# Kernel tuning notes

Hardware: AMD Instinct MI355X
Metric: run time of the kernel (lower is better)

The kernel has to match this reference:

```python
import jax, jax.numpy as jnp
import numpy as np

D = 768
N_GROUPS = 4
KEYS_PER_Q = 4 * 196  # 784


def setup_inputs() -> dict:
    key = jax.random.key(0)
    ks = jax.random.split(key, 6)
    scale = 0.02
    return {
        "LR_image": jax.random.normal(ks[0], (N_GROUPS, 32, D), jnp.float32),
        "HR_image": jax.random.normal(ks[1], (N_GROUPS, 32 * KEYS_PER_Q, D), jnp.float32),
        "Wq": jax.random.normal(ks[2], (D, D), jnp.float32) * scale,
        "bq": jnp.zeros((D,), jnp.float32),
        "Wk": jax.random.normal(ks[3], (D, D), jnp.float32) * scale,
        "bk": jnp.zeros((D,), jnp.float32),
        "Wv": jax.random.normal(ks[4], (D, D), jnp.float32) * scale,
        "bv": jnp.zeros((D,), jnp.float32),
        "Wo": jax.random.normal(ks[5], (D, D), jnp.float32) * scale,
        "bo": jnp.zeros((D,), jnp.float32),
        "gamma": jnp.ones((D,), jnp.float32),
        "beta": jnp.zeros((D,), jnp.float32),
    }


def reference(LR_image, HR_image, Wq, bq, Wk, bk, Wv, bv, Wo, bo, gamma, beta):
    d = LR_image.shape[-1]
    # version == 2 reshapes from the original forward
    lr = LR_image.reshape(1, -1, 32, 1, d)            # [1, N, 32, 1, D]
    hr = HR_image.reshape(1, -1, 32, KEYS_PER_Q, d)   # [1, N, 32, 784, D]
    q = lr @ Wq.T + bq                                # [1, N, 32, 1, D]
    k = hr @ Wk.T + bk                                # [1, N, 32, 784, D]
    v = hr @ Wv.T + bv
    # single-head attention; query_len == 1, key_len == 784
    scores = jnp.einsum('bnsqd,bnskd->bnsqk', q, k) / jnp.sqrt(jnp.float32(d))
    p = jax.nn.softmax(scores, axis=-1)               # dropout = identity (eval)
    x = jnp.einsum('bnsqk,bnskd->bnsqd', p, v)        # [1, N, 32, 1, D]
    x = x.reshape(1, -1, d)                           # [1, N*32, D]
    q = q.reshape(1, -1, d)
    x = x @ Wo.T + bo
    y = q + x                                         # residual (dropout_2 = identity)
    mu = jnp.mean(y, axis=-1, keepdims=True)
    var = jnp.mean((y - mu) ** 2, axis=-1, keepdims=True)
    return (y - mu) * jax.lax.rsqrt(var + 1e-5) * gamma + beta
```

## Files before the change

kernel.cpp:

```cpp
#include <hip/hip_runtime.h>
#include <math.h>

#define D 768
#define DF2 384
#define DF4 192
#define NQ 128
#define KPQ 784
#define NCHUNK 16
#define KCHUNK 49

#define EXP2F(x) __builtin_amdgcn_exp2f(x)

__device__ __forceinline__ float dot4f(const float4 a, const float4 b) {
    return a.x * b.x + a.y * b.y + a.z * b.z + a.w * b.w;
}

__global__ __launch_bounds__(256) void k_tr(const float* __restrict__ Wq,
                                            const float* __restrict__ Wv,
                                            const float* __restrict__ Wo,
                                            float* __restrict__ WqT,
                                            float* __restrict__ WvT,
                                            float* __restrict__ WoT) {
    __shared__ float t[64][65];
    const float* src;
    float* dst;
    if (blockIdx.y == 0)      { src = Wq; dst = WqT; }
    else if (blockIdx.y == 1) { src = Wv; dst = WvT; }
    else                      { src = Wo; dst = WoT; }
    const int tr = blockIdx.x / 12, tc = blockIdx.x % 12;
    const int r0 = tr * 64, c0 = tc * 64;
    const int lr = threadIdx.x >> 6, lc = threadIdx.x & 63;
#pragma unroll
    for (int i = 0; i < 16; ++i)
        t[lr + i * 4][lc] = src[(size_t)(r0 + lr + i * 4) * D + c0 + lc];
    __syncthreads();
#pragma unroll
    for (int i = 0; i < 16; ++i)
        dst[(size_t)(c0 + lr + i * 4) * D + r0 + lc] = t[lc][lr + i * 4];
}

template <bool BIAS, bool RES>
__global__ __launch_bounds__(512) void k_gemm2(const float* __restrict__ A,
                                               const float2* __restrict__ W2,
                                               const float2* __restrict__ bias2,
                                               const float2* __restrict__ res2,
                                               float2* __restrict__ Out2) {
    __shared__ float2 part[8][4][64];
    const int ct  = blockIdx.x % 6;
    const int q0  = (blockIdx.x / 6) * 4;
    const int tid = threadIdx.x;
    const int ds  = __builtin_amdgcn_readfirstlane(tid >> 6);
    const int c2  = tid & 63;
    const int e2  = ct * 64 + c2;
    const float* a0 = A + (size_t)q0 * D;
    const float* a1 = a0 + D;
    const float* a2 = a1 + D;
    const float* a3 = a2 + D;
    float2 acc0 = {0.f, 0.f}, acc1 = {0.f, 0.f}, acc2 = {0.f, 0.f}, acc3 = {0.f, 0.f};
    const int dbase = ds * 96;
#pragma unroll 8
    for (int i = 0; i < 96; ++i) {
        const int d = dbase + i;
        const float2 wv = W2[(size_t)d * DF2 + e2];
        const float x0 = a0[d], x1 = a1[d], x2 = a2[d], x3 = a3[d];
        acc0.x = fmaf(x0, wv.x, acc0.x); acc0.y = fmaf(x0, wv.y, acc0.y);
        acc1.x = fmaf(x1, wv.x, acc1.x); acc1.y = fmaf(x1, wv.y, acc1.y);
        acc2.x = fmaf(x2, wv.x, acc2.x); acc2.y = fmaf(x2, wv.y, acc2.y);
        acc3.x = fmaf(x3, wv.x, acc3.x); acc3.y = fmaf(x3, wv.y, acc3.y);
    }
    part[ds][0][c2] = acc0;
    part[ds][1][c2] = acc1;
    part[ds][2][c2] = acc2;
    part[ds][3][c2] = acc3;
    __syncthreads();
    if (tid < 256) {
        const int q = tid >> 6, c = tid & 63;
        float2 s = {0.f, 0.f};
#pragma unroll
        for (int p = 0; p < 8; ++p) {
            s.x += part[p][q][c].x;
            s.y += part[p][q][c].y;
        }
        if (BIAS) {
            const float2 b = bias2[ct * 64 + c];
            s.x += b.x; s.y += b.y;
        }
        if (RES) {
            const float2 r = res2[(size_t)(q0 + q) * DF2 + ct * 64 + c];
            s.x += r.x; s.y += r.y;
        }
        Out2[(size_t)(q0 + q) * DF2 + ct * 64 + c] = s;
    }
}

__global__ __launch_bounds__(256) void k_flash(const float4* __restrict__ HR,
                                               const float4* __restrict__ qt,
                                               float4* __restrict__ Cpart,
                                               float* __restrict__ Lp) {
    const int b     = blockIdx.x;
    const int qi    = b >> 4;
    const int chunk = b & 15;
    const size_t rowbase = (size_t)qi * KPQ + (size_t)chunk * KCHUNK;
    const int tid  = threadIdx.x;
    const int w    = tid >> 6;
    const int lane = tid & 63;

    const float rsd2 = 0.036084391824351615f * 1.4426950408889634f;
    float4 qa = qt[qi * DF4 + lane];
    float4 qb = qt[qi * DF4 + lane + 64];
    float4 qc = qt[qi * DF4 + lane + 128];
    qa.x *= rsd2; qa.y *= rsd2; qa.z *= rsd2; qa.w *= rsd2;
    qb.x *= rsd2; qb.y *= rsd2; qb.z *= rsd2; qb.w *= rsd2;
    qc.x *= rsd2; qc.y *= rsd2; qc.z *= rsd2; qc.w *= rsd2;

    float l = 0.f;
    float4 c0 = make_float4(0.f, 0.f, 0.f, 0.f);
    float4 c1 = make_float4(0.f, 0.f, 0.f, 0.f);
    float4 c2 = make_float4(0.f, 0.f, 0.f, 0.f);

    int j = w;
    while (j + 4 < KCHUNK) {
        const float4* rowA = HR + (rowbase + (size_t)j) * DF4;
        const float4* rowB = HR + (rowbase + (size_t)(j + 4)) * DF4;
        const float4 a0 = rowA[lane], a1 = rowA[lane + 64], a2 = rowA[lane + 128];
        const float4 b0 = rowB[lane], b1 = rowB[lane + 64], b2 = rowB[lane + 128];
        float p1 = dot4f(qa, a0) + dot4f(qb, a1) + dot4f(qc, a2);
        float p2 = dot4f(qa, b0) + dot4f(qb, b1) + dot4f(qc, b2);
#pragma unroll
        for (int off = 32; off; off >>= 1) {
            p1 += __shfl_xor(p1, off, 64);
            p2 += __shfl_xor(p2, off, 64);
        }
        const float e1 = EXP2F(p1);
        const float e2 = EXP2F(p2);
        l += e1 + e2;
        c0.x += fmaf(e1, a0.x, e2 * b0.x);
        c0.y += fmaf(e1, a0.y, e2 * b0.y);
        c0.z += fmaf(e1, a0.z, e2 * b0.z);
        c0.w += fmaf(e1, a0.w, e2 * b0.w);
        c1.x += fmaf(e1, a1.x, e2 * b1.x);
        c1.y += fmaf(e1, a1.y, e2 * b1.y);
        c1.z += fmaf(e1, a1.z, e2 * b1.z);
        c1.w += fmaf(e1, a1.w, e2 * b1.w);
        c2.x += fmaf(e1, a2.x, e2 * b2.x);
        c2.y += fmaf(e1, a2.y, e2 * b2.y);
        c2.z += fmaf(e1, a2.z, e2 * b2.z);
        c2.w += fmaf(e1, a2.w, e2 * b2.w);
        j += 8;
    }
    if (j < KCHUNK) {
        const float4* rowA = HR + (rowbase + (size_t)j) * DF4;
        const float4 a0 = rowA[lane], a1 = rowA[lane + 64], a2 = rowA[lane + 128];
        float p1 = dot4f(qa, a0) + dot4f(qb, a1) + dot4f(qc, a2);
#pragma unroll
        for (int off = 32; off; off >>= 1) p1 += __shfl_xor(p1, off, 64);
        const float e1 = EXP2F(p1);
        l += e1;
        c0.x = fmaf(e1, a0.x, c0.x); c0.y = fmaf(e1, a0.y, c0.y);
        c0.z = fmaf(e1, a0.z, c0.z); c0.w = fmaf(e1, a0.w, c0.w);
        c1.x = fmaf(e1, a1.x, c1.x); c1.y = fmaf(e1, a1.y, c1.y);
        c1.z = fmaf(e1, a1.z, c1.z); c1.w = fmaf(e1, a1.w, c1.w);
        c2.x = fmaf(e1, a2.x, c2.x); c2.y = fmaf(e1, a2.y, c2.y);
        c2.z = fmaf(e1, a2.z, c2.z); c2.w = fmaf(e1, a2.w, c2.w);
    }

    __shared__ __align__(16) float4 c_lds[4][DF4];
    __shared__ float l_lds[4];
    c_lds[w][lane]       = c0;
    c_lds[w][lane + 64]  = c1;
    c_lds[w][lane + 128] = c2;
    if (lane == 0) l_lds[w] = l;
    __syncthreads();

    if (tid < DF4) {
        float4 cc = make_float4(0.f, 0.f, 0.f, 0.f);
#pragma unroll
        for (int p = 0; p < 4; ++p) {
            const float4 cv = c_lds[p][tid];
            cc.x += cv.x; cc.y += cv.y; cc.z += cv.z; cc.w += cv.w;
        }
        Cpart[(size_t)b * DF4 + tid] = cc;
        if (tid == 0) Lp[b] = l_lds[0] + l_lds[1] + l_lds[2] + l_lds[3];
    }
}

__global__ __launch_bounds__(192) void k_combine(const float4* __restrict__ Cpart,
                                                 const float* __restrict__ Lp,
                                                 float4* __restrict__ Cn) {
    const int qi = blockIdx.x;
    const int f  = threadIdx.x;
    float L = 0.f;
#pragma unroll
    for (int p = 0; p < NCHUNK; ++p) L += Lp[qi * NCHUNK + p];
    float4 c = make_float4(0.f, 0.f, 0.f, 0.f);
#pragma unroll
    for (int p = 0; p < NCHUNK; ++p) {
        const float4 v = Cpart[(size_t)(qi * NCHUNK + p) * DF4 + f];
        c.x += v.x; c.y += v.y; c.z += v.z; c.w += v.w;
    }
    const float inv = 1.f / L;
    c.x *= inv; c.y *= inv; c.z *= inv; c.w *= inv;
    Cn[(size_t)qi * DF4 + f] = c;
}

__global__ __launch_bounds__(256) void k_ln(const float* __restrict__ y,
                                            const float* __restrict__ gamma,
                                            const float* __restrict__ beta,
                                            float* __restrict__ out) {
    __shared__ float sp[4], ssp[4];
    const int qi = blockIdx.x;
    const int tid = threadIdx.x, w = tid >> 6, lane = tid & 63;
    const float* yr = y + (size_t)qi * D;
    const float v0 = yr[tid], v1 = yr[tid + 256], v2 = yr[tid + 512];
    float s  = v0 + v1 + v2;
    float ss = v0 * v0 + v1 * v1 + v2 * v2;
#pragma unroll
    for (int off = 32; off; off >>= 1) {
        s  += __shfl_xor(s, off, 64);
        ss += __shfl_xor(ss, off, 64);
    }
    if (lane == 0) { sp[w] = s; ssp[w] = ss; }
    __syncthreads();
    s  = sp[0] + sp[1] + sp[2] + sp[3];
    ss = ssp[0] + ssp[1] + ssp[2] + ssp[3];
    const float mu  = s * (1.f / 768.f);
    const float var = ss * (1.f / 768.f) - mu * mu;
    const float rs  = rsqrtf(var + 1e-5f);
    float* o = out + (size_t)qi * D;
    o[tid]       = (v0 - mu) * rs * gamma[tid]       + beta[tid];
    o[tid + 256] = (v1 - mu) * rs * gamma[tid + 256] + beta[tid + 256];
    o[tid + 512] = (v2 - mu) * rs * gamma[tid + 512] + beta[tid + 512];
}

extern "C" void kernel_launch(void* const* d_in, const int* in_sizes, int n_in,
                              void* d_out, int out_size, void* d_ws, size_t ws_size,
                              hipStream_t stream) {
    const float* LR    = (const float*)d_in[0];
    const float* HR    = (const float*)d_in[1];
    const float* Wq    = (const float*)d_in[2];
    const float* bq    = (const float*)d_in[3];
    const float* Wk    = (const float*)d_in[4];
    const float* Wv    = (const float*)d_in[6];
    const float* bv    = (const float*)d_in[7];
    const float* Wo    = (const float*)d_in[8];
    const float* bo    = (const float*)d_in[9];
    const float* gamma = (const float*)d_in[10];
    const float* beta  = (const float*)d_in[11];
    float* out = (float*)d_out;

    float* ws = (float*)d_ws;
    float* WqT   = ws;
    float* WvT   = ws + 589824;
    float* WoT   = ws + 1179648;
    float* qbuf  = ws + 1769472;
    float* qtbuf = ws + 1867776;
    float* Cpart = ws + 1966080;
    float* Lp    = ws + 3538944;
    float* Cn    = ws + 3540992;
    float* Xbuf  = ws + 3639296;
    float* ybuf  = ws + 3737600;

    k_tr<<<dim3(144, 3), 256, 0, stream>>>(Wq, Wv, Wo, WqT, WvT, WoT);
    k_gemm2<true, false><<<192, 512, 0, stream>>>(LR, (const float2*)WqT,
                                                  (const float2*)bq, nullptr,
                                                  (float2*)qbuf);
    k_gemm2<false, false><<<192, 512, 0, stream>>>(qbuf, (const float2*)Wk,
                                                   nullptr, nullptr,
                                                   (float2*)qtbuf);
    k_flash<<<NQ * NCHUNK, 256, 0, stream>>>((const float4*)HR, (const float4*)qtbuf,
                                             (float4*)Cpart, Lp);
    k_combine<<<NQ, 192, 0, stream>>>((const float4*)Cpart, Lp, (float4*)Cn);
    k_gemm2<true, false><<<192, 512, 0, stream>>>(Cn, (const float2*)WvT,
                                                  (const float2*)bv, nullptr,
                                                  (float2*)Xbuf);
    k_gemm2<true, true><<<192, 512, 0, stream>>>(Xbuf, (const float2*)WoT,
                                                 (const float2*)bo, (const float2*)qbuf,
                                                 (float2*)ybuf);
    k_ln<<<NQ, 256, 0, stream>>>(ybuf, gamma, beta, out);
}
```

Measured before the change: 104.5 us.

## Fuse Q and Q·Wk projections, and fold chunk combine into the V GEMM

The Q projection and the Wk projection of q are merged into one kernel. Each column-tile block computes its slice of q and then a split-K partial of q·Wk, and the six partials are summed and scaled inside the flash kernel's prologue. The separate combine kernel is removed: the V-projection GEMM now reduces the chunk partials and sums itself, applying 1/L in its epilogue. This cuts two kernel launches and their intermediate round trips, in exchange for redundant partial reductions across column-tile blocks and extra partial buffers.

```diff
diff --git a/kernel.cpp b/kernel.cpp
--- a/kernel.cpp
+++ b/kernel.cpp
@@ -8,6 +8,7 @@
 #define KPQ 784
 #define NCHUNK 16
 #define KCHUNK 49
+#define NCT 6
 
 #define EXP2F(x) __builtin_amdgcn_exp2f(x)
 
@@ -39,8 +40,264 @@
         dst[(size_t)(c0 + lr + i * 4) * D + r0 + lc] = t[lc][lr + i * 4];
 }
 
-template <bool BIAS, bool RES>
-__global__ __launch_bounds__(512) void k_gemm2(const float* __restrict__ A,
+__global__ __launch_bounds__(512) void k_gqqt(const float* __restrict__ LR,
+                                              const float2* __restrict__ WqT2,
+                                              const float2* __restrict__ bq2,
+                                              const float2* __restrict__ Wk2,
+                                              float* __restrict__ qbuf,
+                                              float2* __restrict__ qtp2) {
+    __shared__ float2 part[8][4][64];
+    const int ct  = blockIdx.x;
+    const int q0  = blockIdx.y * 4;
+    const int tid = threadIdx.x;
+    const int wid = __builtin_amdgcn_readfirstlane(tid >> 6);
+    const int c2  = tid & 63;
+
+    {
+        const int e2 = ct * 64 + c2;
+        const float* a0 = LR + (size_t)q0 * D;
+        const float* a1 = a0 + D;
+        const float* a2 = a1 + D;
+        const float* a3 = a2 + D;
+        float2 acc0 = {0.f, 0.f}, acc1 = {0.f, 0.f}, acc2 = {0.f, 0.f}, acc3 = {0.f, 0.f};
+        const int cbase = wid * 96;
+#pragma unroll 8
+        for (int i = 0; i < 96; ++i) {
+            const int c = cbase + i;
+            const float2 wv = WqT2[(size_t)c * DF2 + e2];
+            const float x0 = a0[c], x1 = a1[c], x2 = a2[c], x3 = a3[c];
+            acc0.x = fmaf(x0, wv.x, acc0.x); acc0.y = fmaf(x0, wv.y, acc0.y);
+            acc1.x = fmaf(x1, wv.x, acc1.x); acc1.y = fmaf(x1, wv.y, acc1.y);
+            acc2.x = fmaf(x2, wv.x, acc2.x); acc2.y = fmaf(x2, wv.y, acc2.y);
+            acc3.x = fmaf(x3, wv.x, acc3.x); acc3.y = fmaf(x3, wv.y, acc3.y);
+        }
+        part[wid][0][c2] = acc0;
+        part[wid][1][c2] = acc1;
+        part[wid][2][c2] = acc2;
+        part[wid][3][c2] = acc3;
+    }
+    __syncthreads();
+    if (tid < 256) {
+        const int q = tid >> 6, c = tid & 63;
+        float2 s = {0.f, 0.f};
+#pragma unroll
+        for (int p = 0; p < 8; ++p) {
+            s.x += part[p][q][c].x;
+            s.y += part[p][q][c].y;
+        }
+        const float2 b = bq2[ct * 64 + c];
+        s.x += b.x; s.y += b.y;
+        *reinterpret_cast<float2*>(&qbuf[(size_t)(q0 + q) * D + (ct * 64 + c) * 2]) = s;
+    }
+    __syncthreads();
+
+    if (wid < 6) {
+        const int ee2 = wid * 64 + (tid & 63);
+        float2 b0 = {0.f, 0.f}, b1 = {0.f, 0.f}, b2 = {0.f, 0.f}, b3 = {0.f, 0.f};
+        const int dbase = ct * 128;
+        for (int i4 = 0; i4 < 32; ++i4) {
+            const int d = dbase + i4 * 4;
+            const float4 x0 = *reinterpret_cast<const float4*>(&qbuf[(size_t)(q0 + 0) * D + d]);
+            const float4 x1 = *reinterpret_cast<const float4*>(&qbuf[(size_t)(q0 + 1) * D + d]);
+            const float4 x2 = *reinterpret_cast<const float4*>(&qbuf[(size_t)(q0 + 2) * D + d]);
+            const float4 x3 = *reinterpret_cast<const float4*>(&qbuf[(size_t)(q0 + 3) * D + d]);
+#pragma unroll
+            for (int k = 0; k < 4; ++k) {
+                const float2 wv = Wk2[(size_t)(d + k) * DF2 + ee2];
+                const float v0 = (k == 0) ? x0.x : (k == 1) ? x0.y : (k == 2) ? x0.z : x0.w;
+                const float v1 = (k == 0) ? x1.x : (k == 1) ? x1.y : (k == 2) ? x1.z : x1.w;
+                const float v2 = (k == 0) ? x2.x : (k == 1) ? x2.y : (k == 2) ? x2.z : x2.w;
+                const float v3 = (k == 0) ? x3.x : (k == 1) ? x3.y : (k == 2) ? x3.z : x3.w;
+                b0.x = fmaf(v0, wv.x, b0.x); b0.y = fmaf(v0, wv.y, b0.y);
+                b1.x = fmaf(v1, wv.x, b1.x); b1.y = fmaf(v1, wv.y, b1.y);
+                b2.x = fmaf(v2, wv.x, b2.x); b2.y = fmaf(v2, wv.y, b2.y);
+                b3.x = fmaf(v3, wv.x, b3.x); b3.y = fmaf(v3, wv.y, b3.y);
+            }
+        }
+        qtp2[(size_t)(ct * NQ + q0 + 0) * DF2 + ee2] = b0;
+        qtp2[(size_t)(ct * NQ + q0 + 1) * DF2 + ee2] = b1;
+        qtp2[(size_t)(ct * NQ + q0 + 2) * DF2 + ee2] = b2;
+        qtp2[(size_t)(ct * NQ + q0 + 3) * DF2 + ee2] = b3;
+    }
+}
+
+__global__ __launch_bounds__(256) void k_flash(const float4* __restrict__ HR,
+                                               const float4* __restrict__ qtp4,
+                                               float4* __restrict__ Cpart,
+                                               float* __restrict__ Lp) {
+    __shared__ __align__(16) float4 qt_lds[DF4];
+    const int b     = blockIdx.x;
+    const int qi    = b >> 4;
+    const int chunk = b & 15;
+    const size_t rowbase = (size_t)qi * KPQ + (size_t)chunk * KCHUNK;
+    const int tid  = threadIdx.x;
+    const int w    = tid >> 6;
+    const int lane = tid & 63;
+
+    if (tid < DF4) {
+        float4 s = make_float4(0.f, 0.f, 0.f, 0.f);
+#pragma unroll
+        for (int ct = 0; ct < NCT; ++ct) {
+            const float4 v = qtp4[(size_t)(ct * NQ + qi) * DF4 + tid];
+            s.x += v.x; s.y += v.y; s.z += v.z; s.w += v.w;
+        }
+        const float rsd2 = 0.036084391824351615f * 1.4426950408889634f;
+        s.x *= rsd2; s.y *= rsd2; s.z *= rsd2; s.w *= rsd2;
+        qt_lds[tid] = s;
+    }
+    __syncthreads();
+
+    const float4 qa = qt_lds[lane];
+    const float4 qb = qt_lds[lane + 64];
+    const float4 qc = qt_lds[lane + 128];
+
+    float l = 0.f;
+    float4 c0 = make_float4(0.f, 0.f, 0.f, 0.f);
+    float4 c1 = make_float4(0.f, 0.f, 0.f, 0.f);
+    float4 c2 = make_float4(0.f, 0.f, 0.f, 0.f);
+
+    int j = w;
+    while (j + 4 < KCHUNK) {
+        const float4* rowA = HR + (rowbase + (size_t)j) * DF4;
+        const float4* rowB = HR + (rowbase + (size_t)(j + 4)) * DF4;
+        const float4 a0 = rowA[lane], a1 = rowA[lane + 64], a2 = rowA[lane + 128];
+        const float4 b0 = rowB[lane], b1 = rowB[lane + 64], b2 = rowB[lane + 128];
+        float p1 = dot4f(qa, a0) + dot4f(qb, a1) + dot4f(qc, a2);
+        float p2 = dot4f(qa, b0) + dot4f(qb, b1) + dot4f(qc, b2);
+#pragma unroll
+        for (int off = 32; off; off >>= 1) {
+            p1 += __shfl_xor(p1, off, 64);
+            p2 += __shfl_xor(p2, off, 64);
+        }
+        const float e1 = EXP2F(p1);
+        const float e2 = EXP2F(p2);
+        l += e1 + e2;
+        c0.x += fmaf(e1, a0.x, e2 * b0.x);
+        c0.y += fmaf(e1, a0.y, e2 * b0.y);
+        c0.z += fmaf(e1, a0.z, e2 * b0.z);
+        c0.w += fmaf(e1, a0.w, e2 * b0.w);
+        c1.x += fmaf(e1, a1.x, e2 * b1.x);
+        c1.y += fmaf(e1, a1.y, e2 * b1.y);
+        c1.z += fmaf(e1, a1.z, e2 * b1.z);
+        c1.w += fmaf(e1, a1.w, e2 * b1.w);
+        c2.x += fmaf(e1, a2.x, e2 * b2.x);
+        c2.y += fmaf(e1, a2.y, e2 * b2.y);
+        c2.z += fmaf(e1, a2.z, e2 * b2.z);
+        c2.w += fmaf(e1, a2.w, e2 * b2.w);
+        j += 8;
+    }
+    if (j < KCHUNK) {
+        const float4* rowA = HR + (rowbase + (size_t)j) * DF4;
+        const float4 a0 = rowA[lane], a1 = rowA[lane + 64], a2 = rowA[lane + 128];
+        float p1 = dot4f(qa, a0) + dot4f(qb, a1) + dot4f(qc, a2);
+#pragma unroll
+        for (int off = 32; off; off >>= 1) p1 += __shfl_xor(p1, off, 64);
+        const float e1 = EXP2F(p1);
+        l += e1;
+        c0.x = fmaf(e1, a0.x, c0.x); c0.y = fmaf(e1, a0.y, c0.y);
+        c0.z = fmaf(e1, a0.z, c0.z); c0.w = fmaf(e1, a0.w, c0.w);
+        c1.x = fmaf(e1, a1.x, c1.x); c1.y = fmaf(e1, a1.y, c1.y);
+        c1.z = fmaf(e1, a1.z, c1.z); c1.w = fmaf(e1, a1.w, c1.w);
+        c2.x = fmaf(e1, a2.x, c2.x); c2.y = fmaf(e1, a2.y, c2.y);
+        c2.z = fmaf(e1, a2.z, c2.z); c2.w = fmaf(e1, a2.w, c2.w);
+    }
+
+    __shared__ __align__(16) float4 c_lds[4][DF4];
+    __shared__ float l_lds[4];
+    c_lds[w][lane]       = c0;
+    c_lds[w][lane + 64]  = c1;
+    c_lds[w][lane + 128] = c2;
+    if (lane == 0) l_lds[w] = l;
+    __syncthreads();
+
+    if (tid < DF4) {
+        float4 cc = make_float4(0.f, 0.f, 0.f, 0.f);
+#pragma unroll
+        for (int p = 0; p < 4; ++p) {
+            const float4 cv = c_lds[p][tid];
+            cc.x += cv.x; cc.y += cv.y; cc.z += cv.z; cc.w += cv.w;
+        }
+        Cpart[(size_t)b * DF4 + tid] = cc;
+        if (tid == 0) Lp[b] = l_lds[0] + l_lds[1] + l_lds[2] + l_lds[3];
+    }
+}
+
+__global__ __launch_bounds__(512) void k_gemmV(const float4* __restrict__ Cpart4,
+                                               const float* __restrict__ Lp,
+                                               const float2* __restrict__ WvT2,
+                                               const float2* __restrict__ bv2,
+                                               float* __restrict__ cnbuf,
+                                               float2* __restrict__ Xbuf2) {
+    __shared__ float2 part[8][4][64];
+    const int ct  = blockIdx.x;
+    const int q0  = blockIdx.y * 4;
+    const int tid = threadIdx.x;
+
+    for (int f = tid; f < 4 * DF4; f += 512) {
+        const int q = f / DF4, ff = f % DF4;
+        float4 s = make_float4(0.f, 0.f, 0.f, 0.f);
+#pragma unroll
+        for (int p = 0; p < NCHUNK; ++p) {
+            const float4 v = Cpart4[(size_t)((q0 + q) * NCHUNK + p) * DF4 + ff];
+            s.x += v.x; s.y += v.y; s.z += v.z; s.w += v.w;
+        }
+        *reinterpret_cast<float4*>(&cnbuf[(size_t)(q0 + q) * D + ff * 4]) = s;
+    }
+    float invL[4];
+#pragma unroll
+    for (int q = 0; q < 4; ++q) {
+        float L = 0.f;
+#pragma unroll
+        for (int p = 0; p < NCHUNK; ++p) L += Lp[(q0 + q) * NCHUNK + p];
+        invL[q] = 1.f / L;
+    }
+    __syncthreads();
+
+    const int wid = __builtin_amdgcn_readfirstlane(tid >> 6);
+    const int c2  = tid & 63;
+    const int e2  = ct * 64 + c2;
+    float2 acc0 = {0.f, 0.f}, acc1 = {0.f, 0.f}, acc2 = {0.f, 0.f}, acc3 = {0.f, 0.f};
+    const int dbase = wid * 96;
+    for (int i4 = 0; i4 < 24; ++i4) {
+        const int d = dbase + i4 * 4;
+        const float4 x0 = *reinterpret_cast<const float4*>(&cnbuf[(size_t)(q0 + 0) * D + d]);
+        const float4 x1 = *reinterpret_cast<const float4*>(&cnbuf[(size_t)(q0 + 1) * D + d]);
+        const float4 x2 = *reinterpret_cast<const float4*>(&cnbuf[(size_t)(q0 + 2) * D + d]);
+        const float4 x3 = *reinterpret_cast<const float4*>(&cnbuf[(size_t)(q0 + 3) * D + d]);
+#pragma unroll
+        for (int k = 0; k < 4; ++k) {
+            const float2 wv = WvT2[(size_t)(d + k) * DF2 + e2];
+            const float v0 = (k == 0) ? x0.x : (k == 1) ? x0.y : (k == 2) ? x0.z : x0.w;
+            const float v1 = (k == 0) ? x1.x : (k == 1) ? x1.y : (k == 2) ? x1.z : x1.w;
+            const float v2 = (k == 0) ? x2.x : (k == 1) ? x2.y : (k == 2) ? x2.z : x2.w;
+            const float v3 = (k == 0) ? x3.x : (k == 1) ? x3.y : (k == 2) ? x3.z : x3.w;
+            acc0.x = fmaf(v0, wv.x, acc0.x); acc0.y = fmaf(v0, wv.y, acc0.y);
+            acc1.x = fmaf(v1, wv.x, acc1.x); acc1.y = fmaf(v1, wv.y, acc1.y);
+            acc2.x = fmaf(v2, wv.x, acc2.x); acc2.y = fmaf(v2, wv.y, acc2.y);
+            acc3.x = fmaf(v3, wv.x, acc3.x); acc3.y = fmaf(v3, wv.y, acc3.y);
+        }
+    }
+    part[wid][0][c2] = acc0;
+    part[wid][1][c2] = acc1;
+    part[wid][2][c2] = acc2;
+    part[wid][3][c2] = acc3;
+    __syncthreads();
+    if (tid < 256) {
+        const int q = tid >> 6, c = tid & 63;
+        float2 s = {0.f, 0.f};
+#pragma unroll
+        for (int p = 0; p < 8; ++p) {
+            s.x += part[p][q][c].x;
+            s.y += part[p][q][c].y;
+        }
+        const float2 b = bv2[ct * 64 + c];
+        s.x = s.x * invL[q] + b.x;
+        s.y = s.y * invL[q] + b.y;
+        Xbuf2[(size_t)(q0 + q) * DF2 + ct * 64 + c] = s;
+    }
+}
+
+__global__ __launch_bounds__(512) void k_gemmO(const float* __restrict__ A,
                                                const float2* __restrict__ W2,
                                                const float2* __restrict__ bias2,
                                                const float2* __restrict__ res2,
@@ -81,126 +338,12 @@
             s.x += part[p][q][c].x;
             s.y += part[p][q][c].y;
         }
-        if (BIAS) {
-            const float2 b = bias2[ct * 64 + c];
-            s.x += b.x; s.y += b.y;
-        }
-        if (RES) {
-            const float2 r = res2[(size_t)(q0 + q) * DF2 + ct * 64 + c];
-            s.x += r.x; s.y += r.y;
-        }
+        const float2 b = bias2[ct * 64 + c];
+        const float2 r = res2[(size_t)(q0 + q) * DF2 + ct * 64 + c];
+        s.x += b.x + r.x;
+        s.y += b.y + r.y;
         Out2[(size_t)(q0 + q) * DF2 + ct * 64 + c] = s;
     }
-}
-
-__global__ __launch_bounds__(256) void k_flash(const float4* __restrict__ HR,
-                                               const float4* __restrict__ qt,
-                                               float4* __restrict__ Cpart,
-                                               float* __restrict__ Lp) {
-    const int b     = blockIdx.x;
-    const int qi    = b >> 4;
-    const int chunk = b & 15;
-    const size_t rowbase = (size_t)qi * KPQ + (size_t)chunk * KCHUNK;
-    const int tid  = threadIdx.x;
-    const int w    = tid >> 6;
-    const int lane = tid & 63;
-
-    const float rsd2 = 0.036084391824351615f * 1.4426950408889634f;
-    float4 qa = qt[qi * DF4 + lane];
-    float4 qb = qt[qi * DF4 + lane + 64];
-    float4 qc = qt[qi * DF4 + lane + 128];
-    qa.x *= rsd2; qa.y *= rsd2; qa.z *= rsd2; qa.w *= rsd2;
-    qb.x *= rsd2; qb.y *= rsd2; qb.z *= rsd2; qb.w *= rsd2;
-    qc.x *= rsd2; qc.y *= rsd2; qc.z *= rsd2; qc.w *= rsd2;
-
-    float l = 0.f;
-    float4 c0 = make_float4(0.f, 0.f, 0.f, 0.f);
-    float4 c1 = make_float4(0.f, 0.f, 0.f, 0.f);
-    float4 c2 = make_float4(0.f, 0.f, 0.f, 0.f);
-
-    int j = w;
-    while (j + 4 < KCHUNK) {
-        const float4* rowA = HR + (rowbase + (size_t)j) * DF4;
-        const float4* rowB = HR + (rowbase + (size_t)(j + 4)) * DF4;
-        const float4 a0 = rowA[lane], a1 = rowA[lane + 64], a2 = rowA[lane + 128];
-        const float4 b0 = rowB[lane], b1 = rowB[lane + 64], b2 = rowB[lane + 128];
-        float p1 = dot4f(qa, a0) + dot4f(qb, a1) + dot4f(qc, a2);
-        float p2 = dot4f(qa, b0) + dot4f(qb, b1) + dot4f(qc, b2);
-#pragma unroll
-        for (int off = 32; off; off >>= 1) {
-            p1 += __shfl_xor(p1, off, 64);
-            p2 += __shfl_xor(p2, off, 64);
-        }
-        const float e1 = EXP2F(p1);
-        const float e2 = EXP2F(p2);
-        l += e1 + e2;
-        c0.x += fmaf(e1, a0.x, e2 * b0.x);
-        c0.y += fmaf(e1, a0.y, e2 * b0.y);
-        c0.z += fmaf(e1, a0.z, e2 * b0.z);
-        c0.w += fmaf(e1, a0.w, e2 * b0.w);
-        c1.x += fmaf(e1, a1.x, e2 * b1.x);
-        c1.y += fmaf(e1, a1.y, e2 * b1.y);
-        c1.z += fmaf(e1, a1.z, e2 * b1.z);
-        c1.w += fmaf(e1, a1.w, e2 * b1.w);
-        c2.x += fmaf(e1, a2.x, e2 * b2.x);
-        c2.y += fmaf(e1, a2.y, e2 * b2.y);
-        c2.z += fmaf(e1, a2.z, e2 * b2.z);
-        c2.w += fmaf(e1, a2.w, e2 * b2.w);
-        j += 8;
-    }
-    if (j < KCHUNK) {
-        const float4* rowA = HR + (rowbase + (size_t)j) * DF4;
-        const float4 a0 = rowA[lane], a1 = rowA[lane + 64], a2 = rowA[lane + 128];
-        float p1 = dot4f(qa, a0) + dot4f(qb, a1) + dot4f(qc, a2);
-#pragma unroll
-        for (int off = 32; off; off >>= 1) p1 += __shfl_xor(p1, off, 64);
-        const float e1 = EXP2F(p1);
-        l += e1;
-        c0.x = fmaf(e1, a0.x, c0.x); c0.y = fmaf(e1, a0.y, c0.y);
-        c0.z = fmaf(e1, a0.z, c0.z); c0.w = fmaf(e1, a0.w, c0.w);
-        c1.x = fmaf(e1, a1.x, c1.x); c1.y = fmaf(e1, a1.y, c1.y);
-        c1.z = fmaf(e1, a1.z, c1.z); c1.w = fmaf(e1, a1.w, c1.w);
-        c2.x = fmaf(e1, a2.x, c2.x); c2.y = fmaf(e1, a2.y, c2.y);
-        c2.z = fmaf(e1, a2.z, c2.z); c2.w = fmaf(e1, a2.w, c2.w);
-    }
-
-    __shared__ __align__(16) float4 c_lds[4][DF4];
-    __shared__ float l_lds[4];
-    c_lds[w][lane]       = c0;
-    c_lds[w][lane + 64]  = c1;
-    c_lds[w][lane + 128] = c2;
-    if (lane == 0) l_lds[w] = l;
-    __syncthreads();
-
-    if (tid < DF4) {
-        float4 cc = make_float4(0.f, 0.f, 0.f, 0.f);
-#pragma unroll
-        for (int p = 0; p < 4; ++p) {
-            const float4 cv = c_lds[p][tid];
-            cc.x += cv.x; cc.y += cv.y; cc.z += cv.z; cc.w += cv.w;
-        }
-        Cpart[(size_t)b * DF4 + tid] = cc;
-        if (tid == 0) Lp[b] = l_lds[0] + l_lds[1] + l_lds[2] + l_lds[3];
-    }
-}
-
-__global__ __launch_bounds__(192) void k_combine(const float4* __restrict__ Cpart,
-                                                 const float* __restrict__ Lp,
-                                                 float4* __restrict__ Cn) {
-    const int qi = blockIdx.x;
-    const int f  = threadIdx.x;
-    float L = 0.f;
-#pragma unroll
-    for (int p = 0; p < NCHUNK; ++p) L += Lp[qi * NCHUNK + p];
-    float4 c = make_float4(0.f, 0.f, 0.f, 0.f);
-#pragma unroll
-    for (int p = 0; p < NCHUNK; ++p) {
-        const float4 v = Cpart[(size_t)(qi * NCHUNK + p) * DF4 + f];
-        c.x += v.x; c.y += v.y; c.z += v.z; c.w += v.w;
-    }
-    const float inv = 1.f / L;
-    c.x *= inv; c.y *= inv; c.z *= inv; c.w *= inv;
-    Cn[(size_t)qi * DF4 + f] = c;
 }
 
 __global__ __launch_bounds__(256) void k_ln(const float* __restrict__ y,
@@ -253,28 +396,22 @@
     float* WvT   = ws + 589824;
     float* WoT   = ws + 1179648;
     float* qbuf  = ws + 1769472;
-    float* qtbuf = ws + 1867776;
-    float* Cpart = ws + 1966080;
-    float* Lp    = ws + 3538944;
-    float* Cn    = ws + 3540992;
-    float* Xbuf  = ws + 3639296;
-    float* ybuf  = ws + 3737600;
+    float* qtp   = ws + 1867776;
+    float* Cpart = ws + 2457600;
+    float* Lp    = ws + 4030464;
+    float* cnbuf = ws + 4032512;
+    float* Xbuf  = ws + 4130816;
+    float* ybuf  = ws + 4229120;
 
     k_tr<<<dim3(144, 3), 256, 0, stream>>>(Wq, Wv, Wo, WqT, WvT, WoT);
-    k_gemm2<true, false><<<192, 512, 0, stream>>>(LR, (const float2*)WqT,
-                                                  (const float2*)bq, nullptr,
-                                                  (float2*)qbuf);
-    k_gemm2<false, false><<<192, 512, 0, stream>>>(qbuf, (const float2*)Wk,
-                                                   nullptr, nullptr,
-                                                   (float2*)qtbuf);
-    k_flash<<<NQ * NCHUNK, 256, 0, stream>>>((const float4*)HR, (const float4*)qtbuf,
+    k_gqqt<<<dim3(NCT, 32), 512, 0, stream>>>(LR, (const float2*)WqT, (const float2*)bq,
+                                              (const float2*)Wk, qbuf, (float2*)qtp);
+    k_flash<<<NQ * NCHUNK, 256, 0, stream>>>((const float4*)HR, (const float4*)qtp,
                                              (float4*)Cpart, Lp);
-    k_combine<<<NQ, 192, 0, stream>>>((const float4*)Cpart, Lp, (float4*)Cn);
-    k_gemm2<true, false><<<192, 512, 0, stream>>>(Cn, (const float2*)WvT,
-                                                  (const float2*)bv, nullptr,
-                                                  (float2*)Xbuf);
-    k_gemm2<true, true><<<192, 512, 0, stream>>>(Xbuf, (const float2*)WoT,
-                                                 (const float2*)bo, (const float2*)qbuf,
-                                                 (float2*)ybuf);
+    k_gemmV<<<dim3(NCT, 32), 512, 0, stream>>>((const float4*)Cpart, Lp,
+                                               (const float2*)WvT, (const float2*)bv,
+                                               cnbuf, (float2*)Xbuf);
+    k_gemmO<<<192, 512, 0, stream>>>(Xbuf, (const float2*)WoT, (const float2*)bo,
+                                     (const float2*)qbuf, (float2*)ybuf);
     k_ln<<<NQ, 256, 0, stream>>>(ybuf, gamma, beta, out);
 }
```

After: 122.8 us. 1.18x slower.

## Fuse combine into flash and layernorm into output GEMM via last-block atomics

Applied to the files above, without the earlier changes.

Removes the separate combine and layernorm kernel launches. The last flash block to finish a query now sums the chunk partials, and the last output-GEMM block for a query group runs layernorm, each detected with an atomic counter. The counters are zeroed by the first GEMM launch. This saves two launches and their inter-kernel gaps, at the cost of threadfences, atomics and a serialized tail in the last-arriving blocks.

```diff
diff --git a/kernel.cpp b/kernel.cpp
--- a/kernel.cpp
+++ b/kernel.cpp
@@ -44,10 +44,192 @@
                                                const float2* __restrict__ W2,
                                                const float2* __restrict__ bias2,
                                                const float2* __restrict__ res2,
-                                               float2* __restrict__ Out2) {
+                                               float2* __restrict__ Out2,
+                                               int* zcnt) {
     __shared__ float2 part[8][4][64];
     const int ct  = blockIdx.x % 6;
     const int q0  = (blockIdx.x / 6) * 4;
+    const int tid = threadIdx.x;
+    if (zcnt != nullptr && blockIdx.x == 0 && tid < 160) zcnt[tid] = 0;
+    const int ds  = __builtin_amdgcn_readfirstlane(tid >> 6);
+    const int c2  = tid & 63;
+    const int e2  = ct * 64 + c2;
+    const float* a0 = A + (size_t)q0 * D;
+    const float* a1 = a0 + D;
+    const float* a2 = a1 + D;
+    const float* a3 = a2 + D;
+    float2 acc0 = {0.f, 0.f}, acc1 = {0.f, 0.f}, acc2 = {0.f, 0.f}, acc3 = {0.f, 0.f};
+    const int dbase = ds * 96;
+#pragma unroll 8
+    for (int i = 0; i < 96; ++i) {
+        const int d = dbase + i;
+        const float2 wv = W2[(size_t)d * DF2 + e2];
+        const float x0 = a0[d], x1 = a1[d], x2 = a2[d], x3 = a3[d];
+        acc0.x = fmaf(x0, wv.x, acc0.x); acc0.y = fmaf(x0, wv.y, acc0.y);
+        acc1.x = fmaf(x1, wv.x, acc1.x); acc1.y = fmaf(x1, wv.y, acc1.y);
+        acc2.x = fmaf(x2, wv.x, acc2.x); acc2.y = fmaf(x2, wv.y, acc2.y);
+        acc3.x = fmaf(x3, wv.x, acc3.x); acc3.y = fmaf(x3, wv.y, acc3.y);
+    }
+    part[ds][0][c2] = acc0;
+    part[ds][1][c2] = acc1;
+    part[ds][2][c2] = acc2;
+    part[ds][3][c2] = acc3;
+    __syncthreads();
+    if (tid < 256) {
+        const int q = tid >> 6, c = tid & 63;
+        float2 s = {0.f, 0.f};
+#pragma unroll
+        for (int p = 0; p < 8; ++p) {
+            s.x += part[p][q][c].x;
+            s.y += part[p][q][c].y;
+        }
+        if (BIAS) {
+            const float2 b = bias2[ct * 64 + c];
+            s.x += b.x; s.y += b.y;
+        }
+        if (RES) {
+            const float2 r = res2[(size_t)(q0 + q) * DF2 + ct * 64 + c];
+            s.x += r.x; s.y += r.y;
+        }
+        Out2[(size_t)(q0 + q) * DF2 + ct * 64 + c] = s;
+    }
+}
+
+__global__ __launch_bounds__(256) void k_flash(const float4* __restrict__ HR,
+                                               const float4* __restrict__ qt,
+                                               float4* __restrict__ Cpart,
+                                               float* __restrict__ Lp,
+                                               int* __restrict__ cnt,
+                                               float4* __restrict__ Cn) {
+    const int b     = blockIdx.x;
+    const int qi    = b >> 4;
+    const int chunk = b & 15;
+    const size_t rowbase = (size_t)qi * KPQ + (size_t)chunk * KCHUNK;
+    const int tid  = threadIdx.x;
+    const int w    = tid >> 6;
+    const int lane = tid & 63;
+
+    const float rsd2 = 0.036084391824351615f * 1.4426950408889634f;
+    float4 qa = qt[qi * DF4 + lane];
+    float4 qb = qt[qi * DF4 + lane + 64];
+    float4 qc = qt[qi * DF4 + lane + 128];
+    qa.x *= rsd2; qa.y *= rsd2; qa.z *= rsd2; qa.w *= rsd2;
+    qb.x *= rsd2; qb.y *= rsd2; qb.z *= rsd2; qb.w *= rsd2;
+    qc.x *= rsd2; qc.y *= rsd2; qc.z *= rsd2; qc.w *= rsd2;
+
+    float l = 0.f;
+    float4 c0 = make_float4(0.f, 0.f, 0.f, 0.f);
+    float4 c1 = make_float4(0.f, 0.f, 0.f, 0.f);
+    float4 c2 = make_float4(0.f, 0.f, 0.f, 0.f);
+
+    int j = w;
+    while (j + 4 < KCHUNK) {
+        const float4* rowA = HR + (rowbase + (size_t)j) * DF4;
+        const float4* rowB = HR + (rowbase + (size_t)(j + 4)) * DF4;
+        const float4 a0 = rowA[lane], a1 = rowA[lane + 64], a2 = rowA[lane + 128];
+        const float4 b0 = rowB[lane], b1 = rowB[lane + 64], b2 = rowB[lane + 128];
+        float p1 = dot4f(qa, a0) + dot4f(qb, a1) + dot4f(qc, a2);
+        float p2 = dot4f(qa, b0) + dot4f(qb, b1) + dot4f(qc, b2);
+#pragma unroll
+        for (int off = 32; off; off >>= 1) {
+            p1 += __shfl_xor(p1, off, 64);
+            p2 += __shfl_xor(p2, off, 64);
+        }
+        const float e1 = EXP2F(p1);
+        const float e2 = EXP2F(p2);
+        l += e1 + e2;
+        c0.x += fmaf(e1, a0.x, e2 * b0.x);
+        c0.y += fmaf(e1, a0.y, e2 * b0.y);
+        c0.z += fmaf(e1, a0.z, e2 * b0.z);
+        c0.w += fmaf(e1, a0.w, e2 * b0.w);
+        c1.x += fmaf(e1, a1.x, e2 * b1.x);
+        c1.y += fmaf(e1, a1.y, e2 * b1.y);
+        c1.z += fmaf(e1, a1.z, e2 * b1.z);
+        c1.w += fmaf(e1, a1.w, e2 * b1.w);
+        c2.x += fmaf(e1, a2.x, e2 * b2.x);
+        c2.y += fmaf(e1, a2.y, e2 * b2.y);
+        c2.z += fmaf(e1, a2.z, e2 * b2.z);
+        c2.w += fmaf(e1, a2.w, e2 * b2.w);
+        j += 8;
+    }
+    if (j < KCHUNK) {
+        const float4* rowA = HR + (rowbase + (size_t)j) * DF4;
+        const float4 a0 = rowA[lane], a1 = rowA[lane + 64], a2 = rowA[lane + 128];
+        float p1 = dot4f(qa, a0) + dot4f(qb, a1) + dot4f(qc, a2);
+#pragma unroll
+        for (int off = 32; off; off >>= 1) p1 += __shfl_xor(p1, off, 64);
+        const float e1 = EXP2F(p1);
+        l += e1;
+        c0.x = fmaf(e1, a0.x, c0.x); c0.y = fmaf(e1, a0.y, c0.y);
+        c0.z = fmaf(e1, a0.z, c0.z); c0.w = fmaf(e1, a0.w, c0.w);
+        c1.x = fmaf(e1, a1.x, c1.x); c1.y = fmaf(e1, a1.y, c1.y);
+        c1.z = fmaf(e1, a1.z, c1.z); c1.w = fmaf(e1, a1.w, c1.w);
+        c2.x = fmaf(e1, a2.x, c2.x); c2.y = fmaf(e1, a2.y, c2.y);
+        c2.z = fmaf(e1, a2.z, c2.z); c2.w = fmaf(e1, a2.w, c2.w);
+    }
+
+    __shared__ __align__(16) float4 c_lds[4][DF4];
+    __shared__ float l_lds[4];
+    __shared__ int flag;
+    c_lds[w][lane]       = c0;
+    c_lds[w][lane + 64]  = c1;
+    c_lds[w][lane + 128] = c2;
+    if (lane == 0) l_lds[w] = l;
+    __syncthreads();
+
+    if (tid < DF4) {
+        float4 cc = make_float4(0.f, 0.f, 0.f, 0.f);
+#pragma unroll
+        for (int p = 0; p < 4; ++p) {
+            const float4 cv = c_lds[p][tid];
+            cc.x += cv.x; cc.y += cv.y; cc.z += cv.z; cc.w += cv.w;
+        }
+        Cpart[(size_t)b * DF4 + tid] = cc;
+        if (tid == 0) Lp[b] = l_lds[0] + l_lds[1] + l_lds[2] + l_lds[3];
+    }
+    __syncthreads();
+
+    if (tid == 0) {
+        __threadfence();
+        const int old = atomicAdd(&cnt[qi], 1);
+        flag = (old == NCHUNK - 1) ? 1 : 0;
+    }
+    __syncthreads();
+    if (flag) {
+        __threadfence();
+        if (tid < DF4) {
+            float L = 0.f;
+#pragma unroll
+            for (int p = 0; p < NCHUNK; ++p) L += Lp[qi * NCHUNK + p];
+            float4 c = make_float4(0.f, 0.f, 0.f, 0.f);
+#pragma unroll
+            for (int p = 0; p < NCHUNK; ++p) {
+                const float4 v = Cpart[(size_t)(qi * NCHUNK + p) * DF4 + tid];
+                c.x += v.x; c.y += v.y; c.z += v.z; c.w += v.w;
+            }
+            const float inv = 1.f / L;
+            c.x *= inv; c.y *= inv; c.z *= inv; c.w *= inv;
+            Cn[(size_t)qi * DF4 + tid] = c;
+        }
+    }
+}
+
+__global__ __launch_bounds__(512) void k_gemmO(const float* __restrict__ A,
+                                               const float2* __restrict__ W2,
+                                               const float2* __restrict__ bias2,
+                                               const float2* __restrict__ res2,
+                                               float2* __restrict__ Out2,
+                                               float* __restrict__ ybuf,
+                                               const float* __restrict__ gamma,
+                                               const float* __restrict__ beta,
+                                               float* __restrict__ out,
+                                               int* __restrict__ cnt2) {
+    __shared__ float2 part[8][4][64];
+    __shared__ float sred[8], ssred[8];
+    __shared__ int flag;
+    const int ct  = blockIdx.x % 6;
+    const int qg  = blockIdx.x / 6;
+    const int q0  = qg * 4;
     const int tid = threadIdx.x;
     const int ds  = __builtin_amdgcn_readfirstlane(tid >> 6);
     const int c2  = tid & 63;
@@ -81,155 +263,53 @@
             s.x += part[p][q][c].x;
             s.y += part[p][q][c].y;
         }
-        if (BIAS) {
-            const float2 b = bias2[ct * 64 + c];
-            s.x += b.x; s.y += b.y;
-        }
-        if (RES) {
-            const float2 r = res2[(size_t)(q0 + q) * DF2 + ct * 64 + c];
-            s.x += r.x; s.y += r.y;
-        }
+        const float2 b = bias2[ct * 64 + c];
+        const float2 r = res2[(size_t)(q0 + q) * DF2 + ct * 64 + c];
+        s.x += b.x + r.x;
+        s.y += b.y + r.y;
         Out2[(size_t)(q0 + q) * DF2 + ct * 64 + c] = s;
     }
-}
-
-__global__ __launch_bounds__(256) void k_flash(const float4* __restrict__ HR,
-                                               const float4* __restrict__ qt,
-                                               float4* __restrict__ Cpart,
-                                               float* __restrict__ Lp) {
-    const int b     = blockIdx.x;
-    const int qi    = b >> 4;
-    const int chunk = b & 15;
-    const size_t rowbase = (size_t)qi * KPQ + (size_t)chunk * KCHUNK;
-    const int tid  = threadIdx.x;
-    const int w    = tid >> 6;
-    const int lane = tid & 63;
-
-    const float rsd2 = 0.036084391824351615f * 1.4426950408889634f;
-    float4 qa = qt[qi * DF4 + lane];
-    float4 qb = qt[qi * DF4 + lane + 64];
-    float4 qc = qt[qi * DF4 + lane + 128];
-    qa.x *= rsd2; qa.y *= rsd2; qa.z *= rsd2; qa.w *= rsd2;
-    qb.x *= rsd2; qb.y *= rsd2; qb.z *= rsd2; qb.w *= rsd2;
-    qc.x *= rsd2; qc.y *= rsd2; qc.z *= rsd2; qc.w *= rsd2;
-
-    float l = 0.f;
-    float4 c0 = make_float4(0.f, 0.f, 0.f, 0.f);
-    float4 c1 = make_float4(0.f, 0.f, 0.f, 0.f);
-    float4 c2 = make_float4(0.f, 0.f, 0.f, 0.f);
-
-    int j = w;
-    while (j + 4 < KCHUNK) {
-        const float4* rowA = HR + (rowbase + (size_t)j) * DF4;
-        const float4* rowB = HR + (rowbase + (size_t)(j + 4)) * DF4;
-        const float4 a0 = rowA[lane], a1 = rowA[lane + 64], a2 = rowA[lane + 128];
-        const float4 b0 = rowB[lane], b1 = rowB[lane + 64], b2 = rowB[lane + 128];
-        float p1 = dot4f(qa, a0) + dot4f(qb, a1) + dot4f(qc, a2);
-        float p2 = dot4f(qa, b0) + dot4f(qb, b1) + dot4f(qc, b2);
+    __syncthreads();
+
+    if (tid == 0) {
+        __threadfence();
+        const int old = atomicAdd(&cnt2[qg], 1);
+        flag = (old == 5) ? 1 : 0;
+    }
+    __syncthreads();
+    if (flag) {
+        __threadfence();
+        const int r  = tid >> 7;
+        const int t  = tid & 127;
+        const float* yr = ybuf + (size_t)(q0 + r) * D;
+        float v[6];
+        float s = 0.f, ss = 0.f;
+#pragma unroll
+        for (int k = 0; k < 6; ++k) {
+            v[k] = yr[t + 128 * k];
+            s += v[k];
+            ss += v[k] * v[k];
+        }
 #pragma unroll
         for (int off = 32; off; off >>= 1) {
-            p1 += __shfl_xor(p1, off, 64);
-            p2 += __shfl_xor(p2, off, 64);
-        }
-        const float e1 = EXP2F(p1);
-        const float e2 = EXP2F(p2);
-        l += e1 + e2;
-        c0.x += fmaf(e1, a0.x, e2 * b0.x);
-        c0.y += fmaf(e1, a0.y, e2 * b0.y);
-        c0.z += fmaf(e1, a0.z, e2 * b0.z);
-        c0.w += fmaf(e1, a0.w, e2 * b0.w);
-        c1.x += fmaf(e1, a1.x, e2 * b1.x);
-        c1.y += fmaf(e1, a1.y, e2 * b1.y);
-        c1.z += fmaf(e1, a1.z, e2 * b1.z);
-        c1.w += fmaf(e1, a1.w, e2 * b1.w);
-        c2.x += fmaf(e1, a2.x, e2 * b2.x);
-        c2.y += fmaf(e1, a2.y, e2 * b2.y);
-        c2.z += fmaf(e1, a2.z, e2 * b2.z);
-        c2.w += fmaf(e1, a2.w, e2 * b2.w);
-        j += 8;
-    }
-    if (j < KCHUNK) {
-        const float4* rowA = HR + (rowbase + (size_t)j) * DF4;
-        const float4 a0 = rowA[lane], a1 = rowA[lane + 64], a2 = rowA[lane + 128];
-        float p1 = dot4f(qa, a0) + dot4f(qb, a1) + dot4f(qc, a2);
-#pragma unroll
-        for (int off = 32; off; off >>= 1) p1 += __shfl_xor(p1, off, 64);
-        const float e1 = EXP2F(p1);
-        l += e1;
-        c0.x = fmaf(e1, a0.x, c0.x); c0.y = fmaf(e1, a0.y, c0.y);
-        c0.z = fmaf(e1, a0.z, c0.z); c0.w = fmaf(e1, a0.w, c0.w);
-        c1.x = fmaf(e1, a1.x, c1.x); c1.y = fmaf(e1, a1.y, c1.y);
-        c1.z = fmaf(e1, a1.z, c1.z); c1.w = fmaf(e1, a1.w, c1.w);
-        c2.x = fmaf(e1, a2.x, c2.x); c2.y = fmaf(e1, a2.y, c2.y);
-        c2.z = fmaf(e1, a2.z, c2.z); c2.w = fmaf(e1, a2.w, c2.w);
-    }
-
-    __shared__ __align__(16) float4 c_lds[4][DF4];
-    __shared__ float l_lds[4];
-    c_lds[w][lane]       = c0;
-    c_lds[w][lane + 64]  = c1;
-    c_lds[w][lane + 128] = c2;
-    if (lane == 0) l_lds[w] = l;
-    __syncthreads();
-
-    if (tid < DF4) {
-        float4 cc = make_float4(0.f, 0.f, 0.f, 0.f);
-#pragma unroll
-        for (int p = 0; p < 4; ++p) {
-            const float4 cv = c_lds[p][tid];
-            cc.x += cv.x; cc.y += cv.y; cc.z += cv.z; cc.w += cv.w;
-        }
-        Cpart[(size_t)b * DF4 + tid] = cc;
-        if (tid == 0) Lp[b] = l_lds[0] + l_lds[1] + l_lds[2] + l_lds[3];
-    }
-}
-
-__global__ __launch_bounds__(192) void k_combine(const float4* __restrict__ Cpart,
-                                                 const float* __restrict__ Lp,
-                                                 float4* __restrict__ Cn) {
-    const int qi = blockIdx.x;
-    const int f  = threadIdx.x;
-    float L = 0.f;
-#pragma unroll
-    for (int p = 0; p < NCHUNK; ++p) L += Lp[qi * NCHUNK + p];
-    float4 c = make_float4(0.f, 0.f, 0.f, 0.f);
-#pragma unroll
-    for (int p = 0; p < NCHUNK; ++p) {
-        const float4 v = Cpart[(size_t)(qi * NCHUNK + p) * DF4 + f];
-        c.x += v.x; c.y += v.y; c.z += v.z; c.w += v.w;
-    }
-    const float inv = 1.f / L;
-    c.x *= inv; c.y *= inv; c.z *= inv; c.w *= inv;
-    Cn[(size_t)qi * DF4 + f] = c;
-}
-
-__global__ __launch_bounds__(256) void k_ln(const float* __restrict__ y,
-                                            const float* __restrict__ gamma,
-                                            const float* __restrict__ beta,
-                                            float* __restrict__ out) {
-    __shared__ float sp[4], ssp[4];
-    const int qi = blockIdx.x;
-    const int tid = threadIdx.x, w = tid >> 6, lane = tid & 63;
-    const float* yr = y + (size_t)qi * D;
-    const float v0 = yr[tid], v1 = yr[tid + 256], v2 = yr[tid + 512];
-    float s  = v0 + v1 + v2;
-    float ss = v0 * v0 + v1 * v1 + v2 * v2;
-#pragma unroll
-    for (int off = 32; off; off >>= 1) {
-        s  += __shfl_xor(s, off, 64);
-        ss += __shfl_xor(ss, off, 64);
-    }
-    if (lane == 0) { sp[w] = s; ssp[w] = ss; }
-    __syncthreads();
-    s  = sp[0] + sp[1] + sp[2] + sp[3];
-    ss = ssp[0] + ssp[1] + ssp[2] + ssp[3];
-    const float mu  = s * (1.f / 768.f);
-    const float var = ss * (1.f / 768.f) - mu * mu;
-    const float rs  = rsqrtf(var + 1e-5f);
-    float* o = out + (size_t)qi * D;
-    o[tid]       = (v0 - mu) * rs * gamma[tid]       + beta[tid];
-    o[tid + 256] = (v1 - mu) * rs * gamma[tid + 256] + beta[tid + 256];
-    o[tid + 512] = (v2 - mu) * rs * gamma[tid + 512] + beta[tid + 512];
+            s  += __shfl_xor(s, off, 64);
+            ss += __shfl_xor(ss, off, 64);
+        }
+        const int wv_ = tid >> 6;
+        if ((tid & 63) == 0) { sred[wv_] = s; ssred[wv_] = ss; }
+        __syncthreads();
+        s  = sred[r * 2]  + sred[r * 2 + 1];
+        ss = ssred[r * 2] + ssred[r * 2 + 1];
+        const float mu  = s * (1.f / 768.f);
+        const float var = ss * (1.f / 768.f) - mu * mu;
+        const float rs  = rsqrtf(var + 1e-5f);
+        float* o = out + (size_t)(q0 + r) * D;
+#pragma unroll
+        for (int k = 0; k < 6; ++k) {
+            const int col = t + 128 * k;
+            o[col] = (v[k] - mu) * rs * gamma[col] + beta[col];
+        }
+    }
 }
 
 extern "C" void kernel_launch(void* const* d_in, const int* in_sizes, int n_in,
@@ -256,25 +336,24 @@
     float* qtbuf = ws + 1867776;
     float* Cpart = ws + 1966080;
     float* Lp    = ws + 3538944;
-    float* Cn    = ws + 3540992;
-    float* Xbuf  = ws + 3639296;
-    float* ybuf  = ws + 3737600;
+    int*   cnt   = (int*)(ws + 3540992);
+    float* Cn    = ws + 3541248;
+    float* Xbuf  = ws + 3639552;
+    float* ybuf  = ws + 3737856;
 
     k_tr<<<dim3(144, 3), 256, 0, stream>>>(Wq, Wv, Wo, WqT, WvT, WoT);
     k_gemm2<true, false><<<192, 512, 0, stream>>>(LR, (const float2*)WqT,
                                                   (const float2*)bq, nullptr,
-                                                  (float2*)qbuf);
+                                                  (float2*)qbuf, cnt);
     k_gemm2<false, false><<<192, 512, 0, stream>>>(qbuf, (const float2*)Wk,
                                                    nullptr, nullptr,
-                                                   (float2*)qtbuf);
+                                                   (float2*)qtbuf, nullptr);
     k_flash<<<NQ * NCHUNK, 256, 0, stream>>>((const float4*)HR, (const float4*)qtbuf,
-                                             (float4*)Cpart, Lp);
-    k_combine<<<NQ, 192, 0, stream>>>((const float4*)Cpart, Lp, (float4*)Cn);
+                                             (float4*)Cpart, Lp, cnt, (float4*)Cn);
     k_gemm2<true, false><<<192, 512, 0, stream>>>(Cn, (const float2*)WvT,
                                                   (const float2*)bv, nullptr,
-                                                  (float2*)Xbuf);
-    k_gemm2<true, true><<<192, 512, 0, stream>>>(Xbuf, (const float2*)WoT,
-                                                 (const float2*)bo, (const float2*)qbuf,
-                                                 (float2*)ybuf);
-    k_ln<<<NQ, 256, 0, stream>>>(ybuf, gamma, beta, out);
-}
+                                                  (float2*)Xbuf, nullptr);
+    k_gemmO<<<192, 512, 0, stream>>>(Xbuf, (const float2*)WoT, (const float2*)bo,
+                                     (const float2*)qbuf, (float2*)ybuf, ybuf,
+                                     gamma, beta, out, cnt + 128);
+}
```

After: 310.9 us. 2.97x slower.
